# Kernel tuning notes

Measured on AMD Instinct MI355X. Metric: run time of the kernel, lower is better.

Reference implementation:

```python
import jax, jax.numpy as jnp
import numpy as np

B, N, D = 64, 5000, 128
EPS = 1e-5

def setup_inputs() -> dict:
    key = jax.random.key(0)
    ks = jax.random.split(key, 10)
    s = 1.0 / np.sqrt(D)
    s2 = 1.0 / np.sqrt(2 * D)
    return {
        "batch_size": B,
        "num_customers": N,
        "solution_neighbours": jax.random.randint(ks[0], (B, N, 2), 0, N + 1),
        "embeddings": jax.random.normal(ks[1], (B, N + 1, D), dtype=jnp.float32),
        "w_left": jax.random.uniform(ks[2], (D, D), jnp.float32, -s, s),
        "w_right": jax.random.uniform(ks[3], (D, D), jnp.float32, -s, s),
        "w_comb": jax.random.uniform(ks[4], (D, 2 * D), jnp.float32, -s2, s2),
        "b_comb": jax.random.uniform(ks[5], (D,), jnp.float32, -s2, s2),
        "w_ff": jax.random.uniform(ks[6], (D, D), jnp.float32, -s, s),
        "b_ff": jax.random.uniform(ks[7], (D,), jnp.float32, -s, s),
        "norm_w": jnp.ones((D,), jnp.float32),
        "norm_b": jnp.zeros((D,), jnp.float32),
    }

def _gather(emb, idx):
    # emb: (B, N+1, D), idx: (B, N) -> (B, N, D)
    d = emb.shape[-1]
    return jnp.take_along_axis(emb, jnp.broadcast_to(idx[:, :, None], idx.shape + (d,)), axis=1)

def reference(batch_size, num_customers, solution_neighbours, embeddings,
              w_left, w_right, w_comb, b_comb, w_ff, b_ff, norm_w, norm_b):
    left = _gather(embeddings, solution_neighbours[:, :, 0])
    right = _gather(embeddings, solution_neighbours[:, :, 1])
    # per-edge linear projections (directed graph: separate weights)
    info = left @ w_left.T + right @ w_right.T        # (B, N, D)
    cust = embeddings[:, 1:]                           # (B, N, D)
    combined = jnp.concatenate([cust, info], axis=2)   # (B, N, 2D)
    h = jax.nn.relu(combined @ w_comb.T + b_comb)
    h = h @ w_ff.T + b_ff
    # residual + InstanceNorm1d over the customer axis (per batch, per channel)
    added = cust + h
    mean = jnp.mean(added, axis=1, keepdims=True)
    var = jnp.mean(jnp.square(added - mean), axis=1, keepdims=True)  # biased var
    normed = (added - mean) * jax.lax.rsqrt(var + EPS) * norm_w + norm_b
    return jnp.concatenate([embeddings[:, :1], normed], axis=1)
```

## Files before the change

kernel.cpp:

```cpp
#include <hip/hip_runtime.h>

typedef unsigned short u16;
typedef __attribute__((ext_vector_type(8))) short bf16x8;
typedef __attribute__((ext_vector_type(4))) float f32x4;

#define BB 64
#define NN 5000
#define DD 128
#define EROW 640128
#define CROW 640000
#define NT 79
#define HT 40

#define BAR() do{ asm volatile("s_waitcnt lgkmcnt(0)" ::: "memory"); \
                  __builtin_amdgcn_s_barrier();                      \
                  __builtin_amdgcn_sched_barrier(0); }while(0)

__device__ __forceinline__ u16 f2bf(float f){
  unsigned u = __builtin_bit_cast(unsigned, f);
  u += 0x7fffu + ((u >> 16) & 1u);
  return (u16)(u >> 16);
}
__device__ __forceinline__ float bf2f(u16 h){
  unsigned u = ((unsigned)h) << 16;
  return __builtin_bit_cast(float, u);
}
__device__ __forceinline__ bf16x8 pack8(float4 a, float4 b){
  bf16x8 r;
  r[0] = (short)f2bf(a.x); r[1] = (short)f2bf(a.y);
  r[2] = (short)f2bf(a.z); r[3] = (short)f2bf(a.w);
  r[4] = (short)f2bf(b.x); r[5] = (short)f2bf(b.y);
  r[6] = (short)f2bf(b.z); r[7] = (short)f2bf(b.w);
  return r;
}

__global__ __launch_bounds__(256) void k0_prep(
    const float* __restrict__ wl, const float* __restrict__ wr,
    const float* __restrict__ wcmb, const float* __restrict__ wff,
    const float* __restrict__ emb, float* __restrict__ out,
    u16* __restrict__ wbf, float* __restrict__ sums, float* __restrict__ sumsq)
{
  int t = blockIdx.x * 256 + threadIdx.x;
  if      (t < 16384) wbf[t] = f2bf(wl[t]);
  else if (t < 32768) wbf[t] = f2bf(wr[t - 16384]);
  else if (t < 65536) wbf[t] = f2bf(wcmb[t - 32768]);
  else                wbf[t] = f2bf(wff[t - 65536]);
  if (t < 8192){
    sums[t] = 0.f; sumsq[t] = 0.f;
    int b = t >> 7, d = t & 127;
    out[(size_t)b * EROW + d] = emb[(size_t)b * EROW + d];
  }
}

template<bool BF>
__global__ __launch_bounds__(256, 3)
void k1_main(const int2* __restrict__ sol, const float* __restrict__ emb,
             const u16* __restrict__ wbf, const float* __restrict__ b_comb,
             const float* __restrict__ b_ff, float* __restrict__ out,
             u16* __restrict__ abuf, float* __restrict__ sums, float* __restrict__ sumsq)
{
  const int tid  = threadIdx.x;
  const int lane = tid & 63;
  const int wave = tid >> 6;
  const int q    = lane >> 4;
  const int c    = lane & 15;
  const int b    = blockIdx.y;

  __shared__ u16 A[64][136];
  __shared__ u16 Bb[64][136];

  const float* embB = emb + (size_t)b * EROW;
  const int gi = tid >> 2, gsub = tid & 3;

  const int n0 = wave * 32 + c;
  const int n1 = n0 + 16;

  const u16* wl = wbf;
  const u16* wr = wbf + 16384;
  const u16* wc = wbf + 32768;
  const u16* wf = wbf + 65536;

  const float bc0 = b_comb[n0], bc1 = b_comb[n1];
  const float bf0 = b_ff[n0],  bf1 = b_ff[n1];

  int tile = blockIdx.x;

  float4 pl[8], pr[8];
  {
    int r0 = min(tile * 64 + gi, NN - 1);
    int2 p = sol[(size_t)b * NN + r0];
    const float4* vL = (const float4*)(embB + (size_t)p.x * DD) + gsub * 8;
    const float4* vR = (const float4*)(embB + (size_t)p.y * DD) + gsub * 8;
    #pragma unroll
    for (int j = 0; j < 8; ++j) pl[j] = vL[j];
    #pragma unroll
    for (int j = 0; j < 8; ++j) pr[j] = vR[j];
  }

  const f32x4 fz = {0.f, 0.f, 0.f, 0.f};

  #pragma unroll
  for (int it = 0; it < 2; ++it){
    const int rbase = tile * 64;
    const int RC = min(64, NN - rbase);

    if (it) BAR();

    float4 ca[8];
    {
      int crow = min(rbase + gi + 1, NN);
      const float4* vC = (const float4*)(embB + (size_t)crow * DD) + gsub * 8;
      #pragma unroll
      for (int j = 0; j < 8; ++j) ca[j] = vC[j];
    }
    int2 pnx = {0, 0};
    if (it == 0 && tile + HT < NT){
      int r0 = min((tile + HT) * 64 + gi, NN - 1);
      pnx = sol[(size_t)b * NN + r0];
    }

    #pragma unroll
    for (int j = 0; j < 4; ++j){
      *(bf16x8*)&A [gi][gsub * 32 + j * 8] = pack8(pl[2*j], pl[2*j+1]);
      *(bf16x8*)&Bb[gi][gsub * 32 + j * 8] = pack8(pr[2*j], pr[2*j+1]);
    }
    BAR();

    f32x4 acc[4][2];

    #pragma unroll
    for (int mt = 0; mt < 4; ++mt){ acc[mt][0] = fz; acc[mt][1] = fz; }
    #pragma unroll
    for (int ks = 0; ks < 8; ++ks){
      const u16* W = (ks < 4) ? wl : wr;
      const int kk = (ks & 3) * 32 + q * 8;
      bf16x8 b0 = *(const bf16x8*)(W + n0 * 128 + kk);
      bf16x8 b1 = *(const bf16x8*)(W + n1 * 128 + kk);
      #pragma unroll
      for (int mt = 0; mt < 4; ++mt){
        bf16x8 a = *(const bf16x8*)&((ks < 4) ? A : Bb)[mt * 16 + c][kk];
        acc[mt][0] = __builtin_amdgcn_mfma_f32_16x16x32_bf16(a, b0, acc[mt][0], 0, 0, 0);
        acc[mt][1] = __builtin_amdgcn_mfma_f32_16x16x32_bf16(a, b1, acc[mt][1], 0, 0, 0);
      }
    }
    BAR();

    #pragma unroll
    for (int mt = 0; mt < 4; ++mt){
      #pragma unroll
      for (int r = 0; r < 4; ++r){
        int m = mt * 16 + q * 4 + r;
        A[m][n0] = f2bf(acc[mt][0][r]);
        A[m][n1] = f2bf(acc[mt][1][r]);
      }
    }
    #pragma unroll
    for (int j = 0; j < 4; ++j)
      *(bf16x8*)&Bb[gi][gsub * 32 + j * 8] = pack8(ca[2*j], ca[2*j+1]);
    BAR();

    #pragma unroll
    for (int mt = 0; mt < 4; ++mt){ acc[mt][0] = fz; acc[mt][1] = fz; }
    #pragma unroll
    for (int ks = 0; ks < 8; ++ks){
      const int kk = (ks & 3) * 32 + q * 8;
      const int kg = ks * 32 + q * 8;
      bf16x8 b0 = *(const bf16x8*)(wc + n0 * 256 + kg);
      bf16x8 b1 = *(const bf16x8*)(wc + n1 * 256 + kg);
      #pragma unroll
      for (int mt = 0; mt < 4; ++mt){
        bf16x8 a = *(const bf16x8*)&((ks < 4) ? Bb : A)[mt * 16 + c][kk];
        acc[mt][0] = __builtin_amdgcn_mfma_f32_16x16x32_bf16(a, b0, acc[mt][0], 0, 0, 0);
        acc[mt][1] = __builtin_amdgcn_mfma_f32_16x16x32_bf16(a, b1, acc[mt][1], 0, 0, 0);
      }
    }
    BAR();
    #pragma unroll
    for (int mt = 0; mt < 4; ++mt){
      #pragma unroll
      for (int r = 0; r < 4; ++r){
        int m = mt * 16 + q * 4 + r;
        A[m][n0] = f2bf(fmaxf(acc[mt][0][r] + bc0, 0.f));
        A[m][n1] = f2bf(fmaxf(acc[mt][1][r] + bc1, 0.f));
      }
    }
    BAR();

    #pragma unroll
    for (int mt = 0; mt < 4; ++mt){ acc[mt][0] = fz; acc[mt][1] = fz; }
    #pragma unroll
    for (int ks = 0; ks < 4; ++ks){
      const int kk = ks * 32 + q * 8;
      bf16x8 b0 = *(const bf16x8*)(wf + n0 * 128 + kk);
      bf16x8 b1 = *(const bf16x8*)(wf + n1 * 128 + kk);
      #pragma unroll
      for (int mt = 0; mt < 4; ++mt){
        bf16x8 a = *(const bf16x8*)&A[mt * 16 + c][kk];
        acc[mt][0] = __builtin_amdgcn_mfma_f32_16x16x32_bf16(a, b0, acc[mt][0], 0, 0, 0);
        acc[mt][1] = __builtin_amdgcn_mfma_f32_16x16x32_bf16(a, b1, acc[mt][1], 0, 0, 0);
      }
    }

    __builtin_amdgcn_sched_barrier(0);
    if (it == 0 && tile + HT < NT){
      const float4* vL = (const float4*)(embB + (size_t)pnx.x * DD) + gsub * 8;
      const float4* vR = (const float4*)(embB + (size_t)pnx.y * DD) + gsub * 8;
      #pragma unroll
      for (int j = 0; j < 8; ++j) pl[j] = vL[j];
      #pragma unroll
      for (int j = 0; j < 8; ++j) pr[j] = vR[j];
    }
    __builtin_amdgcn_sched_barrier(0);

    float sv0 = 0.f, sq0 = 0.f, sv1 = 0.f, sq1 = 0.f;
    float* outB = out + (size_t)b * EROW;
    #pragma unroll
    for (int mt = 0; mt < 4; ++mt){
      #pragma unroll
      for (int r = 0; r < 4; ++r){
        int m = mt * 16 + q * 4 + r;
        float v0 = acc[mt][0][r] + bf0 + bf2f(Bb[m][n0]);
        float v1 = acc[mt][1][r] + bf1 + bf2f(Bb[m][n1]);
        acc[mt][0][r] = v0; acc[mt][1][r] = v1;
        if (m < RC){
          sv0 += v0; sq0 += v0 * v0;
          sv1 += v1; sq1 += v1 * v1;
          if (!BF){
            size_t ro = (size_t)(rbase + m + 1) * DD;
            outB[ro + n0] = v0;
            outB[ro + n1] = v1;
          }
        }
      }
    }
    sv0 += __shfl_xor(sv0, 16); sv0 += __shfl_xor(sv0, 32);
    sq0 += __shfl_xor(sq0, 16); sq0 += __shfl_xor(sq0, 32);
    sv1 += __shfl_xor(sv1, 16); sv1 += __shfl_xor(sv1, 32);
    sq1 += __shfl_xor(sq1, 16); sq1 += __shfl_xor(sq1, 32);
    if (q == 0){
      atomicAdd(&sums [b * DD + n0], sv0);
      atomicAdd(&sumsq[b * DD + n0], sq0);
      atomicAdd(&sums [b * DD + n1], sv1);
      atomicAdd(&sumsq[b * DD + n1], sq1);
    }

    if (BF){
      BAR();
      #pragma unroll
      for (int mt = 0; mt < 4; ++mt){
        #pragma unroll
        for (int r = 0; r < 4; ++r){
          int m = mt * 16 + q * 4 + r;
          A[m][n0] = f2bf(acc[mt][0][r]);
          A[m][n1] = f2bf(acc[mt][1][r]);
        }
      }
      BAR();
      const int row = tid >> 2, cb = tid & 3;
      if (rbase + row < NN){
        u16* dst = abuf + ((size_t)b * NN + rbase + row) * DD + cb * 32;
        #pragma unroll
        for (int j = 0; j < 4; ++j)
          *(bf16x8*)(dst + j * 8) = *(const bf16x8*)&A[row][cb * 32 + j * 8];
      }
    }

    tile += HT;
    if (tile >= NT) break;
  }
}

__global__ __launch_bounds__(256) void k2_bf(
    const u16* __restrict__ abuf, const float* __restrict__ sums,
    const float* __restrict__ sumsq, const float* __restrict__ nw,
    const float* __restrict__ nb, float* __restrict__ out)
{
  __shared__ float ssc[128], ssh[128];
  const int b = blockIdx.y;
  const int t = threadIdx.x;
  if (t < 128){
    float mean = sums[b * DD + t] * (1.f / NN);
    float var  = sumsq[b * DD + t] * (1.f / NN) - mean * mean;
    float inv  = rsqrtf(var + 1e-5f);
    float sc   = inv * nw[t];
    ssc[t] = sc;
    ssh[t] = nb[t] - mean * sc;
  }
  __syncthreads();
  const int e = (blockIdx.x * 256 + t) * 8;
  if (e >= CROW) return;
  const int d = e & 127;
  const uint4 raw = *(const uint4*)(abuf + (size_t)b * CROW + e);
  const float4 s0 = *(const float4*)&ssc[d];
  const float4 s1 = *(const float4*)&ssc[d + 4];
  const float4 h0 = *(const float4*)&ssh[d];
  const float4 h1 = *(const float4*)&ssh[d + 4];
  float4 v0, v1;
  v0.x = __builtin_bit_cast(float, raw.x << 16);
  v0.y = __builtin_bit_cast(float, raw.x & 0xffff0000u);
  v0.z = __builtin_bit_cast(float, raw.y << 16);
  v0.w = __builtin_bit_cast(float, raw.y & 0xffff0000u);
  v1.x = __builtin_bit_cast(float, raw.z << 16);
  v1.y = __builtin_bit_cast(float, raw.z & 0xffff0000u);
  v1.z = __builtin_bit_cast(float, raw.w << 16);
  v1.w = __builtin_bit_cast(float, raw.w & 0xffff0000u);
  v0.x = v0.x * s0.x + h0.x; v0.y = v0.y * s0.y + h0.y;
  v0.z = v0.z * s0.z + h0.z; v0.w = v0.w * s0.w + h0.w;
  v1.x = v1.x * s1.x + h1.x; v1.y = v1.y * s1.y + h1.y;
  v1.z = v1.z * s1.z + h1.z; v1.w = v1.w * s1.w + h1.w;
  float4* p = (float4*)(out + (size_t)b * EROW + DD + e);
  p[0] = v0; p[1] = v1;
}

__global__ __launch_bounds__(256) void k2_rmw(
    float* __restrict__ out, const float* __restrict__ sums,
    const float* __restrict__ sumsq, const float* __restrict__ nw,
    const float* __restrict__ nb)
{
  __shared__ float ssc[128], ssh[128];
  const int b = blockIdx.y;
  const int t = threadIdx.x;
  if (t < 128){
    float mean = sums[b * DD + t] * (1.f / NN);
    float var  = sumsq[b * DD + t] * (1.f / NN) - mean * mean;
    float inv  = rsqrtf(var + 1e-5f);
    float sc   = inv * nw[t];
    ssc[t] = sc;
    ssh[t] = nb[t] - mean * sc;
  }
  __syncthreads();
  const int e = (blockIdx.x * 256 + t) * 8;
  if (e >= CROW) return;
  const int d = e & 127;
  const float4 s0 = *(const float4*)&ssc[d];
  const float4 s1 = *(const float4*)&ssc[d + 4];
  const float4 h0 = *(const float4*)&ssh[d];
  const float4 h1 = *(const float4*)&ssh[d + 4];
  float4* p = (float4*)(out + (size_t)b * EROW + DD + e);
  float4 v0 = p[0], v1 = p[1];
  v0.x = v0.x * s0.x + h0.x; v0.y = v0.y * s0.y + h0.y;
  v0.z = v0.z * s0.z + h0.z; v0.w = v0.w * s0.w + h0.w;
  v1.x = v1.x * s1.x + h1.x; v1.y = v1.y * s1.y + h1.y;
  v1.z = v1.z * s1.z + h1.z; v1.w = v1.w * s1.w + h1.w;
  p[0] = v0; p[1] = v1;
}

extern "C" void kernel_launch(void* const* d_in, const int* in_sizes, int n_in,
                              void* d_out, int out_size, void* d_ws, size_t ws_size,
                              hipStream_t stream)
{
  const int2*  sol  = (const int2*) d_in[2];
  const float* emb  = (const float*)d_in[3];
  const float* wl   = (const float*)d_in[4];
  const float* wr   = (const float*)d_in[5];
  const float* wcmb = (const float*)d_in[6];
  const float* bcmb = (const float*)d_in[7];
  const float* wff  = (const float*)d_in[8];
  const float* bff  = (const float*)d_in[9];
  const float* nw   = (const float*)d_in[10];
  const float* nb   = (const float*)d_in[11];
  float* out = (float*)d_out;

  u16*   wbf   = (u16*)d_ws;
  float* sums  = (float*)((char*)d_ws + 163840);
  float* sumsq = (float*)((char*)d_ws + 196608);
  u16*   abuf  = (u16*)((char*)d_ws + 294912);

  const size_t need = 294912ull + (size_t)BB * NN * DD * 2;
  const bool bfpath = (ws_size >= need);

  k0_prep <<<320, 256, 0, stream>>>(wl, wr, wcmb, wff, emb, out, wbf, sums, sumsq);
  if (bfpath){
    k1_main<true> <<<dim3(HT, BB), 256, 0, stream>>>(sol, emb, wbf, bcmb, bff, out, abuf, sums, sumsq);
    k2_bf  <<<dim3(313, 64), 256, 0, stream>>>(abuf, sums, sumsq, nw, nb, out);
  } else {
    k1_main<false><<<dim3(HT, BB), 256, 0, stream>>>(sol, emb, wbf, bcmb, bff, out, abuf, sums, sumsq);
    k2_rmw <<<dim3(313, 64), 256, 0, stream>>>(out, sums, sumsq, nw, nb);
  }
}
```

Baseline: 478.5 us.

## Give each wave independent 32-row tile with register-resident activations, no block barriers

Restructures the main fused kernel so each wave processes its own 32 rows across all 128 output channels. Gathered embeddings become MFMA B-operands held in registers, and weights are streamed as A-operands from global memory. Per-wave LDS scratch replaces the shared block tiles, so workgroup barriers are replaced by LDS waitcnts. The old two-iteration prefetch loop is dropped because each block now covers 128 rows in a single pass. This adds register pressure (launch bounds lowered to 2 waves per SIMD) and many more atomics per block for the norm statistics, and removes the overlap of the next tile's gather.

```diff
diff --git a/kernel.cpp b/kernel.cpp
--- a/kernel.cpp
+++ b/kernel.cpp
@@ -9,12 +9,6 @@
 #define DD 128
 #define EROW 640128
 #define CROW 640000
-#define NT 79
-#define HT 40
-
-#define BAR() do{ asm volatile("s_waitcnt lgkmcnt(0)" ::: "memory"); \
-                  __builtin_amdgcn_s_barrier();                      \
-                  __builtin_amdgcn_sched_barrier(0); }while(0)
 
 __device__ __forceinline__ u16 f2bf(float f){
   unsigned u = __builtin_bit_cast(unsigned, f);
@@ -33,6 +27,9 @@
   r[6] = (short)f2bf(b.z); r[7] = (short)f2bf(b.w);
   return r;
 }
+
+#define LGKM0() do{ asm volatile("s_waitcnt lgkmcnt(0)" ::: "memory"); \
+                    __builtin_amdgcn_sched_barrier(0); }while(0)
 
 __global__ __launch_bounds__(256) void k0_prep(
     const float* __restrict__ wl, const float* __restrict__ wr,
@@ -53,7 +50,7 @@
 }
 
 template<bool BF>
-__global__ __launch_bounds__(256, 3)
+__global__ __launch_bounds__(256, 2)
 void k1_main(const int2* __restrict__ sol, const float* __restrict__ emb,
              const u16* __restrict__ wbf, const float* __restrict__ b_comb,
              const float* __restrict__ b_ff, float* __restrict__ out,
@@ -61,212 +58,236 @@
 {
   const int tid  = threadIdx.x;
   const int lane = tid & 63;
-  const int wave = tid >> 6;
+  const int w    = tid >> 6;
   const int q    = lane >> 4;
   const int c    = lane & 15;
   const int b    = blockIdx.y;
-
-  __shared__ u16 A[64][136];
-  __shared__ u16 Bb[64][136];
+  const int R0   = blockIdx.x * 128 + w * 32;
+
+  __shared__ u16 scr_all[4][32][136];
+  u16 (*scr)[136] = scr_all[w];
 
   const float* embB = emb + (size_t)b * EROW;
-  const int gi = tid >> 2, gsub = tid & 3;
-
-  const int n0 = wave * 32 + c;
-  const int n1 = n0 + 16;
-
   const u16* wl = wbf;
   const u16* wr = wbf + 16384;
   const u16* wc = wbf + 32768;
   const u16* wf = wbf + 65536;
 
-  const float bc0 = b_comb[n0], bc1 = b_comb[n1];
-  const float bf0 = b_ff[n0],  bf1 = b_ff[n1];
-
-  int tile = blockIdx.x;
-
-  float4 pl[8], pr[8];
-  {
-    int r0 = min(tile * 64 + gi, NN - 1);
-    int2 p = sol[(size_t)b * NN + r0];
-    const float4* vL = (const float4*)(embB + (size_t)p.x * DD) + gsub * 8;
-    const float4* vR = (const float4*)(embB + (size_t)p.y * DD) + gsub * 8;
-    #pragma unroll
-    for (int j = 0; j < 8; ++j) pl[j] = vL[j];
-    #pragma unroll
-    for (int j = 0; j < 8; ++j) pr[j] = vR[j];
+  f32x4 bcv[8], bfv[8];
+  #pragma unroll
+  for (int t = 0; t < 8; ++t){
+    bcv[t] = *(const f32x4*)(b_comb + t*16 + q*4);
+    bfv[t] = *(const f32x4*)(b_ff  + t*16 + q*4);
+  }
+
+  int iL[2], iR[2];
+  #pragma unroll
+  for (int mm = 0; mm < 2; ++mm){
+    int r = min(R0 + mm*16 + c, NN - 1);
+    int2 p = sol[(size_t)b * NN + r];
+    iL[mm] = p.x; iR[mm] = p.y;
+  }
+  bf16x8 lF[2][4], rF[2][4];
+  #pragma unroll
+  for (int mm = 0; mm < 2; ++mm){
+    const float* pL = embB + (size_t)iL[mm] * DD + q*8;
+    const float* pR = embB + (size_t)iR[mm] * DD + q*8;
+    #pragma unroll
+    for (int kt = 0; kt < 4; ++kt){
+      float4 a0 = *(const float4*)(pL + kt*32);
+      float4 a1 = *(const float4*)(pL + kt*32 + 4);
+      float4 b0 = *(const float4*)(pR + kt*32);
+      float4 b1 = *(const float4*)(pR + kt*32 + 4);
+      lF[mm][kt] = pack8(a0, a1);
+      rF[mm][kt] = pack8(b0, b1);
+    }
   }
 
   const f32x4 fz = {0.f, 0.f, 0.f, 0.f};
-
-  #pragma unroll
-  for (int it = 0; it < 2; ++it){
-    const int rbase = tile * 64;
-    const int RC = min(64, NN - rbase);
-
-    if (it) BAR();
-
-    float4 ca[8];
-    {
-      int crow = min(rbase + gi + 1, NN);
-      const float4* vC = (const float4*)(embB + (size_t)crow * DD) + gsub * 8;
-      #pragma unroll
-      for (int j = 0; j < 8; ++j) ca[j] = vC[j];
-    }
-    int2 pnx = {0, 0};
-    if (it == 0 && tile + HT < NT){
-      int r0 = min((tile + HT) * 64 + gi, NN - 1);
-      pnx = sol[(size_t)b * NN + r0];
-    }
-
-    #pragma unroll
-    for (int j = 0; j < 4; ++j){
-      *(bf16x8*)&A [gi][gsub * 32 + j * 8] = pack8(pl[2*j], pl[2*j+1]);
-      *(bf16x8*)&Bb[gi][gsub * 32 + j * 8] = pack8(pr[2*j], pr[2*j+1]);
-    }
-    BAR();
-
-    f32x4 acc[4][2];
-
-    #pragma unroll
-    for (int mt = 0; mt < 4; ++mt){ acc[mt][0] = fz; acc[mt][1] = fz; }
-    #pragma unroll
-    for (int ks = 0; ks < 8; ++ks){
-      const u16* W = (ks < 4) ? wl : wr;
-      const int kk = (ks & 3) * 32 + q * 8;
-      bf16x8 b0 = *(const bf16x8*)(W + n0 * 128 + kk);
-      bf16x8 b1 = *(const bf16x8*)(W + n1 * 128 + kk);
-      #pragma unroll
-      for (int mt = 0; mt < 4; ++mt){
-        bf16x8 a = *(const bf16x8*)&((ks < 4) ? A : Bb)[mt * 16 + c][kk];
-        acc[mt][0] = __builtin_amdgcn_mfma_f32_16x16x32_bf16(a, b0, acc[mt][0], 0, 0, 0);
-        acc[mt][1] = __builtin_amdgcn_mfma_f32_16x16x32_bf16(a, b1, acc[mt][1], 0, 0, 0);
+  f32x4 acc[8][2];
+
+  #pragma unroll
+  for (int t = 0; t < 8; ++t){ acc[t][0] = fz; acc[t][1] = fz; }
+  #pragma unroll
+  for (int t = 0; t < 8; ++t){
+    const int wrow = (t*16 + c) * DD + q*8;
+    #pragma unroll
+    for (int kt = 0; kt < 4; ++kt){
+      bf16x8 wlf = *(const bf16x8*)(wl + wrow + kt*32);
+      #pragma unroll
+      for (int mm = 0; mm < 2; ++mm)
+        acc[t][mm] = __builtin_amdgcn_mfma_f32_16x16x32_bf16(wlf, lF[mm][kt], acc[t][mm], 0, 0, 0);
+    }
+    #pragma unroll
+    for (int kt = 0; kt < 4; ++kt){
+      bf16x8 wrf = *(const bf16x8*)(wr + wrow + kt*32);
+      #pragma unroll
+      for (int mm = 0; mm < 2; ++mm)
+        acc[t][mm] = __builtin_amdgcn_mfma_f32_16x16x32_bf16(wrf, rF[mm][kt], acc[t][mm], 0, 0, 0);
+    }
+  }
+
+  #pragma unroll
+  for (int t = 0; t < 8; ++t){
+    #pragma unroll
+    for (int mm = 0; mm < 2; ++mm){
+      ushort4 u;
+      u.x = f2bf(acc[t][mm][0]); u.y = f2bf(acc[t][mm][1]);
+      u.z = f2bf(acc[t][mm][2]); u.w = f2bf(acc[t][mm][3]);
+      *(ushort4*)&scr[mm*16 + c][t*16 + q*4] = u;
+    }
+  }
+
+  bf16x8 cF[2][4];
+  #pragma unroll
+  for (int mm = 0; mm < 2; ++mm){
+    int crow = min(R0 + mm*16 + c + 1, NN);
+    const float* pC = embB + (size_t)crow * DD + q*8;
+    #pragma unroll
+    for (int kt = 0; kt < 4; ++kt){
+      float4 a0 = *(const float4*)(pC + kt*32);
+      float4 a1 = *(const float4*)(pC + kt*32 + 4);
+      cF[mm][kt] = pack8(a0, a1);
+    }
+  }
+
+  LGKM0();
+
+  bf16x8 iF[2][4];
+  #pragma unroll
+  for (int mm = 0; mm < 2; ++mm)
+    #pragma unroll
+    for (int kt = 0; kt < 4; ++kt)
+      iF[mm][kt] = *(const bf16x8*)&scr[mm*16 + c][kt*32 + q*8];
+
+  #pragma unroll
+  for (int t = 0; t < 8; ++t){ acc[t][0] = fz; acc[t][1] = fz; }
+  #pragma unroll
+  for (int t = 0; t < 8; ++t){
+    const int wrow = (t*16 + c) * 256 + q*8;
+    #pragma unroll
+    for (int kt = 0; kt < 4; ++kt){
+      bf16x8 wcf = *(const bf16x8*)(wc + wrow + kt*32);
+      #pragma unroll
+      for (int mm = 0; mm < 2; ++mm)
+        acc[t][mm] = __builtin_amdgcn_mfma_f32_16x16x32_bf16(wcf, cF[mm][kt], acc[t][mm], 0, 0, 0);
+    }
+    #pragma unroll
+    for (int kt = 0; kt < 4; ++kt){
+      bf16x8 wcf = *(const bf16x8*)(wc + wrow + 128 + kt*32);
+      #pragma unroll
+      for (int mm = 0; mm < 2; ++mm)
+        acc[t][mm] = __builtin_amdgcn_mfma_f32_16x16x32_bf16(wcf, iF[mm][kt], acc[t][mm], 0, 0, 0);
+    }
+  }
+
+  #pragma unroll
+  for (int t = 0; t < 8; ++t){
+    #pragma unroll
+    for (int mm = 0; mm < 2; ++mm){
+      ushort4 u;
+      u.x = f2bf(fmaxf(acc[t][mm][0] + bcv[t][0], 0.f));
+      u.y = f2bf(fmaxf(acc[t][mm][1] + bcv[t][1], 0.f));
+      u.z = f2bf(fmaxf(acc[t][mm][2] + bcv[t][2], 0.f));
+      u.w = f2bf(fmaxf(acc[t][mm][3] + bcv[t][3], 0.f));
+      *(ushort4*)&scr[mm*16 + c][t*16 + q*4] = u;
+    }
+  }
+  LGKM0();
+
+  bf16x8 hF[2][4];
+  #pragma unroll
+  for (int mm = 0; mm < 2; ++mm)
+    #pragma unroll
+    for (int kt = 0; kt < 4; ++kt)
+      hF[mm][kt] = *(const bf16x8*)&scr[mm*16 + c][kt*32 + q*8];
+
+  #pragma unroll
+  for (int t = 0; t < 8; ++t){ acc[t][0] = fz; acc[t][1] = fz; }
+  #pragma unroll
+  for (int t = 0; t < 8; ++t){
+    const int wrow = (t*16 + c) * DD + q*8;
+    #pragma unroll
+    for (int kt = 0; kt < 4; ++kt){
+      bf16x8 wff = *(const bf16x8*)(wf + wrow + kt*32);
+      #pragma unroll
+      for (int mm = 0; mm < 2; ++mm)
+        acc[t][mm] = __builtin_amdgcn_mfma_f32_16x16x32_bf16(wff, hF[mm][kt], acc[t][mm], 0, 0, 0);
+    }
+  }
+
+  #pragma unroll
+  for (int mm = 0; mm < 2; ++mm)
+    #pragma unroll
+    for (int kt = 0; kt < 4; ++kt)
+      *(bf16x8*)&scr[mm*16 + c][kt*32 + q*8] = cF[mm][kt];
+  LGKM0();
+
+  const bool ok0 = (R0 + c) < NN;
+  const bool ok1 = (R0 + 16 + c) < NN;
+  float s[8][4], sq[8][4];
+  #pragma unroll
+  for (int t = 0; t < 8; ++t)
+    #pragma unroll
+    for (int r = 0; r < 4; ++r){ s[t][r] = 0.f; sq[t][r] = 0.f; }
+
+  #pragma unroll
+  for (int t = 0; t < 8; ++t){
+    #pragma unroll
+    for (int mm = 0; mm < 2; ++mm){
+      ushort4 cu = *(const ushort4*)&scr[mm*16 + c][t*16 + q*4];
+      float v0 = acc[t][mm][0] + bfv[t][0] + bf2f(cu.x);
+      float v1 = acc[t][mm][1] + bfv[t][1] + bf2f(cu.y);
+      float v2 = acc[t][mm][2] + bfv[t][2] + bf2f(cu.z);
+      float v3 = acc[t][mm][3] + bfv[t][3] + bf2f(cu.w);
+      bool ok = mm ? ok1 : ok0;
+      if (ok){
+        s[t][0] += v0; sq[t][0] += v0*v0;
+        s[t][1] += v1; sq[t][1] += v1*v1;
+        s[t][2] += v2; sq[t][2] += v2*v2;
+        s[t][3] += v3; sq[t][3] += v3*v3;
       }
-    }
-    BAR();
-
-    #pragma unroll
-    for (int mt = 0; mt < 4; ++mt){
+      ushort4 au;
+      au.x = f2bf(v0); au.y = f2bf(v1); au.z = f2bf(v2); au.w = f2bf(v3);
+      *(ushort4*)&scr[mm*16 + c][t*16 + q*4] = au;
+      if (!BF && ok){
+        float4 fv = {v0, v1, v2, v3};
+        *(float4*)(out + (size_t)b * EROW + (size_t)(R0 + mm*16 + c + 1) * DD + t*16 + q*4) = fv;
+      }
+    }
+  }
+
+  #pragma unroll
+  for (int t = 0; t < 8; ++t){
+    #pragma unroll
+    for (int r = 0; r < 4; ++r){
+      float a = s[t][r], d = sq[t][r];
+      a += __shfl_xor(a, 1); a += __shfl_xor(a, 2); a += __shfl_xor(a, 4); a += __shfl_xor(a, 8);
+      d += __shfl_xor(d, 1); d += __shfl_xor(d, 2); d += __shfl_xor(d, 4); d += __shfl_xor(d, 8);
+      s[t][r] = a; sq[t][r] = d;
+    }
+  }
+  if (c == 0){
+    #pragma unroll
+    for (int t = 0; t < 8; ++t){
       #pragma unroll
       for (int r = 0; r < 4; ++r){
-        int m = mt * 16 + q * 4 + r;
-        A[m][n0] = f2bf(acc[mt][0][r]);
-        A[m][n1] = f2bf(acc[mt][1][r]);
+        int n = t*16 + q*4 + r;
+        atomicAdd(&sums [b * DD + n], s[t][r]);
+        atomicAdd(&sumsq[b * DD + n], sq[t][r]);
       }
     }
-    #pragma unroll
-    for (int j = 0; j < 4; ++j)
-      *(bf16x8*)&Bb[gi][gsub * 32 + j * 8] = pack8(ca[2*j], ca[2*j+1]);
-    BAR();
-
-    #pragma unroll
-    for (int mt = 0; mt < 4; ++mt){ acc[mt][0] = fz; acc[mt][1] = fz; }
-    #pragma unroll
-    for (int ks = 0; ks < 8; ++ks){
-      const int kk = (ks & 3) * 32 + q * 8;
-      const int kg = ks * 32 + q * 8;
-      bf16x8 b0 = *(const bf16x8*)(wc + n0 * 256 + kg);
-      bf16x8 b1 = *(const bf16x8*)(wc + n1 * 256 + kg);
-      #pragma unroll
-      for (int mt = 0; mt < 4; ++mt){
-        bf16x8 a = *(const bf16x8*)&((ks < 4) ? Bb : A)[mt * 16 + c][kk];
-        acc[mt][0] = __builtin_amdgcn_mfma_f32_16x16x32_bf16(a, b0, acc[mt][0], 0, 0, 0);
-        acc[mt][1] = __builtin_amdgcn_mfma_f32_16x16x32_bf16(a, b1, acc[mt][1], 0, 0, 0);
-      }
-    }
-    BAR();
-    #pragma unroll
-    for (int mt = 0; mt < 4; ++mt){
-      #pragma unroll
-      for (int r = 0; r < 4; ++r){
-        int m = mt * 16 + q * 4 + r;
-        A[m][n0] = f2bf(fmaxf(acc[mt][0][r] + bc0, 0.f));
-        A[m][n1] = f2bf(fmaxf(acc[mt][1][r] + bc1, 0.f));
-      }
-    }
-    BAR();
-
-    #pragma unroll
-    for (int mt = 0; mt < 4; ++mt){ acc[mt][0] = fz; acc[mt][1] = fz; }
-    #pragma unroll
-    for (int ks = 0; ks < 4; ++ks){
-      const int kk = ks * 32 + q * 8;
-      bf16x8 b0 = *(const bf16x8*)(wf + n0 * 128 + kk);
-      bf16x8 b1 = *(const bf16x8*)(wf + n1 * 128 + kk);
-      #pragma unroll
-      for (int mt = 0; mt < 4; ++mt){
-        bf16x8 a = *(const bf16x8*)&A[mt * 16 + c][kk];
-        acc[mt][0] = __builtin_amdgcn_mfma_f32_16x16x32_bf16(a, b0, acc[mt][0], 0, 0, 0);
-        acc[mt][1] = __builtin_amdgcn_mfma_f32_16x16x32_bf16(a, b1, acc[mt][1], 0, 0, 0);
-      }
-    }
-
-    __builtin_amdgcn_sched_barrier(0);
-    if (it == 0 && tile + HT < NT){
-      const float4* vL = (const float4*)(embB + (size_t)pnx.x * DD) + gsub * 8;
-      const float4* vR = (const float4*)(embB + (size_t)pnx.y * DD) + gsub * 8;
-      #pragma unroll
-      for (int j = 0; j < 8; ++j) pl[j] = vL[j];
-      #pragma unroll
-      for (int j = 0; j < 8; ++j) pr[j] = vR[j];
-    }
-    __builtin_amdgcn_sched_barrier(0);
-
-    float sv0 = 0.f, sq0 = 0.f, sv1 = 0.f, sq1 = 0.f;
-    float* outB = out + (size_t)b * EROW;
-    #pragma unroll
-    for (int mt = 0; mt < 4; ++mt){
-      #pragma unroll
-      for (int r = 0; r < 4; ++r){
-        int m = mt * 16 + q * 4 + r;
-        float v0 = acc[mt][0][r] + bf0 + bf2f(Bb[m][n0]);
-        float v1 = acc[mt][1][r] + bf1 + bf2f(Bb[m][n1]);
-        acc[mt][0][r] = v0; acc[mt][1][r] = v1;
-        if (m < RC){
-          sv0 += v0; sq0 += v0 * v0;
-          sv1 += v1; sq1 += v1 * v1;
-          if (!BF){
-            size_t ro = (size_t)(rbase + m + 1) * DD;
-            outB[ro + n0] = v0;
-            outB[ro + n1] = v1;
-          }
-        }
-      }
-    }
-    sv0 += __shfl_xor(sv0, 16); sv0 += __shfl_xor(sv0, 32);
-    sq0 += __shfl_xor(sq0, 16); sq0 += __shfl_xor(sq0, 32);
-    sv1 += __shfl_xor(sv1, 16); sv1 += __shfl_xor(sv1, 32);
-    sq1 += __shfl_xor(sq1, 16); sq1 += __shfl_xor(sq1, 32);
-    if (q == 0){
-      atomicAdd(&sums [b * DD + n0], sv0);
-      atomicAdd(&sumsq[b * DD + n0], sq0);
-      atomicAdd(&sums [b * DD + n1], sv1);
-      atomicAdd(&sumsq[b * DD + n1], sq1);
-    }
-
-    if (BF){
-      BAR();
-      #pragma unroll
-      for (int mt = 0; mt < 4; ++mt){
-        #pragma unroll
-        for (int r = 0; r < 4; ++r){
-          int m = mt * 16 + q * 4 + r;
-          A[m][n0] = f2bf(acc[mt][0][r]);
-          A[m][n1] = f2bf(acc[mt][1][r]);
-        }
-      }
-      BAR();
-      const int row = tid >> 2, cb = tid & 3;
-      if (rbase + row < NN){
-        u16* dst = abuf + ((size_t)b * NN + rbase + row) * DD + cb * 32;
-        #pragma unroll
-        for (int j = 0; j < 4; ++j)
-          *(bf16x8*)(dst + j * 8) = *(const bf16x8*)&A[row][cb * 32 + j * 8];
-      }
-    }
-
-    tile += HT;
-    if (tile >= NT) break;
+  }
+
+  if (BF){
+    LGKM0();
+    const int row = lane >> 1, half = lane & 1;
+    if (R0 + row < NN){
+      u16* dst = abuf + ((size_t)b * NN + R0 + row) * DD + half*64;
+      #pragma unroll
+      for (int j = 0; j < 8; ++j)
+        *(bf16x8*)(dst + j*8) = *(const bf16x8*)&scr[row][half*64 + j*8];
+    }
   }
 }
 
@@ -371,10 +392,10 @@
 
   k0_prep <<<320, 256, 0, stream>>>(wl, wr, wcmb, wff, emb, out, wbf, sums, sumsq);
   if (bfpath){
-    k1_main<true> <<<dim3(HT, BB), 256, 0, stream>>>(sol, emb, wbf, bcmb, bff, out, abuf, sums, sumsq);
+    k1_main<true> <<<dim3(40, BB), 256, 0, stream>>>(sol, emb, wbf, bcmb, bff, out, abuf, sums, sumsq);
     k2_bf  <<<dim3(313, 64), 256, 0, stream>>>(abuf, sums, sumsq, nw, nb, out);
   } else {
-    k1_main<false><<<dim3(HT, BB), 256, 0, stream>>>(sol, emb, wbf, bcmb, bff, out, abuf, sums, sumsq);
+    k1_main<false><<<dim3(40, BB), 256, 0, stream>>>(sol, emb, wbf, bcmb, bff, out, abuf, sums, sumsq);
     k2_rmw <<<dim3(313, 64), 256, 0, stream>>>(out, sums, sumsq, nw, nb);
   }
 }
```

Result: slower. 692.7 us (+44.8%).
